# Kernel tuning notes

Hardware: AMD Instinct MI355X
Metric: run time of the kernel (lower is better)

The kernel has to match this reference:

```python
import jax, jax.numpy as jnp
import numpy as np

N, K, H, E, HEADS, MULT = 10000, 32, 128, 128, 8, 2
HD = H // HEADS


def _ln(x, g, b):
    m = jnp.mean(x, axis=-1, keepdims=True)
    v = jnp.var(x, axis=-1, keepdims=True)
    return (x - m) * jax.lax.rsqrt(v + 1e-5) * g + b


def setup_inputs() -> dict:
    key = jax.random.key(0)
    ks = jax.random.split(key, 40)
    s = 0.05
    inp = {
        "node_features": jax.random.normal(ks[0], (N, H), jnp.float32),
        "edge_features": jax.random.normal(ks[1], (N, K, H), jnp.float32),
        "edge_attr": jax.random.normal(ks[2], (N, K, E), jnp.float32),
        "neighbor_list": jax.random.randint(ks[3], (N, K), 0, N),
        "num_valid": jax.random.randint(ks[4], (N,), 1, K + 1),
        # edge_linear: E -> H (with activation)
        "W_edge": jax.random.normal(ks[5], (E, H), jnp.float32) * s,
        "b_edge": jnp.zeros((H,), jnp.float32),
        # node_linear: 2H -> H (cat of center + gathered neighbor features)
        "W_node": jax.random.normal(ks[6], (2 * H, H), jnp.float32) * s,
        "b_node": jnp.zeros((H,), jnp.float32),
        # message_linear: 2H -> H
        "W_msg": jax.random.normal(ks[7], (2 * H, H), jnp.float32) * s,
        "b_msg": jnp.zeros((H,), jnp.float32),
        # multi-head attention in/out projections
        "W_qkv": jax.random.normal(ks[8], (H, 3 * H), jnp.float32) * s,
        "b_qkv": jnp.zeros((3 * H,), jnp.float32),
        "W_out": jax.random.normal(ks[9], (H, H), jnp.float32) * s,
        "b_out": jnp.zeros((H,), jnp.float32),
        # layernorms
        "g_attn": jnp.ones((H,), jnp.float32), "be_attn": jnp.zeros((H,), jnp.float32),
        "g_fn": jnp.ones((H,), jnp.float32), "be_fn": jnp.zeros((H,), jnp.float32),
        "g_fe": jnp.ones((H,), jnp.float32), "be_fe": jnp.zeros((H,), jnp.float32),
        # FFNs (node and edge), hidden = MULT*H
        "Wn1": jax.random.normal(ks[10], (H, MULT * H), jnp.float32) * s,
        "bn1": jnp.zeros((MULT * H,), jnp.float32),
        "Wn2": jax.random.normal(ks[11], (MULT * H, H), jnp.float32) * s,
        "bn2": jnp.zeros((H,), jnp.float32),
        "We1": jax.random.normal(ks[12], (H, MULT * H), jnp.float32) * s,
        "be1": jnp.zeros((MULT * H,), jnp.float32),
        "We2": jax.random.normal(ks[13], (MULT * H, H), jnp.float32) * s,
        "be2": jnp.zeros((H,), jnp.float32),
    }
    return inp


def _block(node_features, edge_features, edge_attr, neighbor_list, mask,
           W_edge, b_edge, W_node, b_node, W_msg, b_msg,
           W_qkv, b_qkv, W_out, b_out,
           g_attn, be_attn, g_fn, be_fn, g_fe, be_fe,
           Wn1, bn1, Wn2, bn2, We1, be1, We2, be2):
    act = jax.nn.gelu
    # --- pre-attention norm on nodes ---
    node_hidden = _ln(node_features, g_attn, be_attn)                 # [N,H]
    # --- graph attention: gather -> MLPs -> local windowed attention -> scatter ---
    edge_hidden = act(jnp.einsum('nke,eh->nkh', edge_attr, W_edge) + b_edge)   # [N,K,H]
    nbr = node_hidden[neighbor_list]                                   # [N,K,H] gather
    center = jnp.broadcast_to(node_hidden[:, None, :], nbr.shape)      # [N,K,H]
    node_cat = jnp.concatenate([center, nbr], axis=-1)                 # [N,K,2H]
    node_hid = act(jnp.einsum('nkf,fh->nkh', node_cat, W_node) + b_node)
    msg = act(jnp.einsum('nkf,fh->nkh',
                         jnp.concatenate([edge_hidden, node_hid], axis=-1),
                         W_msg) + b_msg)                               # [N,K,H]
    # multi-head self-attention per node over its K neighbors, key padding mask
    qkv = jnp.einsum('nkh,hf->nkf', msg, W_qkv) + b_qkv                # [N,K,3H]
    q, k, v = jnp.split(qkv, 3, axis=-1)
    q = q.reshape(N, K, HEADS, HD)
    k = k.reshape(N, K, HEADS, HD)
    v = v.reshape(N, K, HEADS, HD)
    scores = jnp.einsum('nqhd,nkhd->nhqk', q, k) / np.sqrt(HD)         # [N,heads,K,K]
    scores = jnp.where(mask[:, None, None, :], scores, jnp.float32(-1e9))
    attn = jax.nn.softmax(scores, axis=-1)
    ctx = jnp.einsum('nhqk,nkhd->nqhd', attn, v).reshape(N, K, H)
    edge_out = jnp.einsum('nkh,hf->nkf', ctx, W_out) + b_out           # [N,K,H]
    # masked scatter-aggregate back to nodes
    node_out = jnp.sum(edge_out * mask[:, :, None], axis=1)            # [N,H]
    # residuals
    node_features = node_out + node_features
    edge_features = edge_out + edge_features
    # --- FFN block ---
    nh = _ln(node_features, g_fn, be_fn)
    eh = _ln(edge_features, g_fe, be_fe)
    nh = act(nh @ Wn1 + bn1) @ Wn2 + bn2
    eh = jnp.einsum('nkf,fh->nkh', act(jnp.einsum('nkh,hf->nkf', eh, We1) + be1), We2) + be2
    return node_features + nh, edge_features + eh


def reference(node_features, edge_features, edge_attr, neighbor_list, num_valid,
              W_edge, b_edge, W_node, b_node, W_msg, b_msg,
              W_qkv, b_qkv, W_out, b_out,
              g_attn, be_attn, g_fn, be_fn, g_fe, be_fe,
              Wn1, bn1, Wn2, bn2, We1, be1, We2, be2):
    mask = jnp.arange(K)[None, :] < num_valid[:, None]                 # [N,K] bool
    return _block(node_features, edge_features, edge_attr, neighbor_list, mask,
                  W_edge, b_edge, W_node, b_node, W_msg, b_msg,
                  W_qkv, b_qkv, W_out, b_out,
                  g_attn, be_attn, g_fn, be_fn, g_fe, be_fe,
                  Wn1, bn1, Wn2, bn2, We1, be1, We2, be2)
```

## Files before the change

### kernel.cpp

```cpp
#include <hip/hip_runtime.h>
#include <hip/hip_bf16.h>
#include <cstddef>

#define N_NODES 10000
#define KNBR 32
#define HDIM 128
#define NHEADS 8

using short8 = __attribute__((ext_vector_type(8))) short;
using short4v = __attribute__((ext_vector_type(4))) short;
using f32x4 = __attribute__((ext_vector_type(4))) float;

__device__ __forceinline__ f32x4 mfma16(short8 a, short8 b, f32x4 c) {
  return __builtin_amdgcn_mfma_f32_16x16x32_bf16(a, b, c, 0, 0, 0);
}

__device__ __forceinline__ short f2bf(float f) {
  __hip_bfloat16 h = __float2bfloat16(f);
  return __builtin_bit_cast(short, h);
}
__device__ __forceinline__ float bf2f(short s) {
  unsigned u = ((unsigned)(unsigned short)s) << 16;
  return __builtin_bit_cast(float, u);
}

__device__ __forceinline__ float gelu_f(float x) {
  float a = 0.7978845608028654f * fmaf(0.044715f * x, x * x, x);
  float e = __expf(2.0f * a);
  return 0.5f * x * (2.0f - 2.0f / (e + 1.0f));
}

__device__ __forceinline__ short4v pack4f(float a, float b, float c, float d) {
  short4v v; v[0] = f2bf(a); v[1] = f2bf(b); v[2] = f2bf(c); v[3] = f2bf(d);
  return v;
}
__device__ __forceinline__ short4v pack_gelu4(f32x4 acc, float4 bb) {
  return pack4f(gelu_f(acc[0] + bb.x), gelu_f(acc[1] + bb.y),
                gelu_f(acc[2] + bb.z), gelu_f(acc[3] + bb.w));
}

__device__ __forceinline__ short8 ld_sw128(const short* b, int r, int ch) {
  return *(const short8*)(b + r * 128 + (((ch ^ (r & 7))) << 3));
}
__device__ __forceinline__ short8 ld_sw256(const short* b, int r, int ch) {
  return *(const short8*)(b + r * 256 + (((ch ^ (r & 7))) << 3));
}
__device__ __forceinline__ void st_sw128(short* b, int r, int col, short v) {
  b[r * 128 + ((((col >> 3) ^ (r & 7))) << 3) + (col & 7)] = v;
}
__device__ __forceinline__ void st_sw128_v4(short* b, int r, int colb, short4v v) {
  *(short4v*)(b + r * 128 + ((((colb >> 3) ^ (r & 7))) << 3) + (colb & 7)) = v;
}
__device__ __forceinline__ void st_sw256_v4(short* b, int r, int colb, short4v v) {
  *(short4v*)(b + r * 256 + ((((colb >> 3) ^ (r & 7))) << 3) + (colb & 7)) = v;
}

template <int MT, int NT, int KS, typename ALoad, typename Epi>
__device__ __forceinline__ void wgemm(ALoad aload, const short* __restrict__ Bt,
                                      Epi epi) {
  const int lane = threadIdx.x & 63;
  const int lm = lane & 15, lq = lane >> 4;
  f32x4 acc[MT][NT];
#pragma unroll
  for (int mt = 0; mt < MT; ++mt)
#pragma unroll
    for (int nt = 0; nt < NT; ++nt) acc[mt][nt] = {0.f, 0.f, 0.f, 0.f};
#pragma unroll
  for (int k = 0; k < KS; ++k) {
    short8 a[MT];
#pragma unroll
    for (int mt = 0; mt < MT; ++mt) a[mt] = aload(mt * 16 + lm, k, lq);
#pragma unroll
    for (int nt = 0; nt < NT; ++nt) {
      short8 b = *(const short8*)(Bt + (nt * 16 + lm) * (KS * 32) + k * 32 + lq * 8);
#pragma unroll
      for (int mt = 0; mt < MT; ++mt) acc[mt][nt] = mfma16(a[mt], b, acc[mt][nt]);
    }
  }
#pragma unroll
  for (int mt = 0; mt < MT; ++mt)
#pragma unroll
    for (int nt = 0; nt < NT; ++nt) epi(mt, nt, acc[mt][nt]);
}

template <int MT, int NT, int KS, typename ALoad, typename Epi>
__device__ __forceinline__ void wgemm_t(ALoad aload, const short* __restrict__ Bt,
                                        Epi epi) {
  const int lane = threadIdx.x & 63;
  const int lm = lane & 15, lq = lane >> 4;
  f32x4 acc[MT][NT];
#pragma unroll
  for (int mt = 0; mt < MT; ++mt)
#pragma unroll
    for (int nt = 0; nt < NT; ++nt) acc[mt][nt] = {0.f, 0.f, 0.f, 0.f};
#pragma unroll
  for (int k = 0; k < KS; ++k) {
    short8 a[MT];
#pragma unroll
    for (int mt = 0; mt < MT; ++mt) a[mt] = aload(mt * 16 + lm, k, lq);
#pragma unroll
    for (int nt = 0; nt < NT; ++nt) {
      short8 b = *(const short8*)(Bt + (nt * 16 + lm) * (KS * 32) + k * 32 + lq * 8);
#pragma unroll
      for (int mt = 0; mt < MT; ++mt) acc[mt][nt] = mfma16(b, a[mt], acc[mt][nt]);
    }
  }
#pragma unroll
  for (int mt = 0; mt < MT; ++mt)
#pragma unroll
    for (int nt = 0; nt < NT; ++nt) epi(mt, nt, acc[mt][nt]);
}

struct WSrc { const float* p[9]; };

__global__ void wprep_kernel(WSrc ws, short* __restrict__ dst) {
  const int cum[10] = {0, 16384, 49152, 81920, 131072, 147456, 180224, 212992, 245760, 278528};
  const int Ks[9] = {128, 256, 256, 128, 128, 128, 256, 128, 256};
  const int Ns[9] = {128, 128, 128, 384, 128, 256, 128, 256, 128};
  int eg = blockIdx.x * 256 + threadIdx.x;
  int id = 0;
#pragma unroll
  for (int i = 0; i < 8; ++i) id += (eg >= cum[i + 1]) ? 1 : 0;
  int e = eg - cum[id];
  int K = Ks[id];
  int n = (K == 128) ? (e >> 7) : (e >> 8);
  int k = e - n * K;
  dst[eg] = f2bf(ws.p[id][k * Ns[id] + n]);
}

__global__ __launch_bounds__(256) void ln_in_kernel(
    const float* __restrict__ in, const float* __restrict__ g,
    const float* __restrict__ be, short* __restrict__ out) {
  __shared__ float scr[32 * 8 * 2 + 64];
  const int tid = threadIdx.x;
  const int r = tid >> 3, j = tid & 7;
  const int base = blockIdx.x * 32;
  const int rg = base + r;
  const bool valid = rg < N_NODES;
  float4 v[4];
#pragma unroll
  for (int i = 0; i < 4; ++i)
    v[i] = valid ? ((const float4*)(in + (size_t)rg * 128 + j * 16))[i]
                 : make_float4(0.f, 0.f, 0.f, 0.f);
  float s = 0.f, s2 = 0.f;
#pragma unroll
  for (int i = 0; i < 4; ++i) {
    s += v[i].x + v[i].y + v[i].z + v[i].w;
    s2 = fmaf(v[i].x, v[i].x, s2); s2 = fmaf(v[i].y, v[i].y, s2);
    s2 = fmaf(v[i].z, v[i].z, s2); s2 = fmaf(v[i].w, v[i].w, s2);
  }
  scr[r * 8 + j] = s;
  scr[256 + r * 8 + j] = s2;
  __syncthreads();
  if (tid < 32) {
    float ss = 0.f, q2 = 0.f;
#pragma unroll
    for (int i = 0; i < 8; ++i) { ss += scr[tid * 8 + i]; q2 += scr[256 + tid * 8 + i]; }
    float mn = ss * (1.f / 128.f);
    float vr = fmaf(-mn, mn, q2 * (1.f / 128.f));
    scr[512 + tid] = mn;
    scr[544 + tid] = rsqrtf(vr + 1e-5f);
  }
  __syncthreads();
  if (!valid) return;
  float mn = scr[512 + r], rs = scr[544 + r];
  short8 o[2];
#pragma unroll
  for (int i = 0; i < 4; ++i) {
    int c0 = j * 16 + i * 4;
    float4 gg = *(const float4*)(g + c0);
    float4 bb = *(const float4*)(be + c0);
    float* vf = (float*)&v[i];
    float* gf = (float*)&gg;
    float* bf = (float*)&bb;
#pragma unroll
    for (int e = 0; e < 4; ++e)
      o[i >> 1][(i & 1) * 4 + e] = f2bf(fmaf((vf[e] - mn) * rs, gf[e], bf[e]));
  }
  *(short8*)(out + (size_t)rg * 128 + j * 16) = o[0];
  *(short8*)(out + (size_t)rg * 128 + j * 16 + 8) = o[1];
}

__global__ __launch_bounds__(256, 3) void egab_main(
    const float* __restrict__ nf, const float* __restrict__ ef,
    const float* __restrict__ ea, const int* __restrict__ nlist,
    const int* __restrict__ nvalid,
    const float* __restrict__ b_edge, const float* __restrict__ b_node,
    const float* __restrict__ b_msg, const float* __restrict__ b_qkv,
    const float* __restrict__ b_out, const float* __restrict__ g_fe,
    const float* __restrict__ be_fe, const float* __restrict__ be1,
    const float* __restrict__ be2,
    const short* __restrict__ WtE, const short* __restrict__ WtN,
    const short* __restrict__ WtM, const short* __restrict__ WtQ,
    const short* __restrict__ WtO, const short* __restrict__ WtE1,
    const short* __restrict__ WtE2, const short* __restrict__ nh_bf,
    float* __restrict__ out_node, float* __restrict__ out_edge) {
  __shared__ short lds[16384];
  short* R0 = lds;
  short* R1 = lds + 4096;
  short* R2 = lds + 8192;
  short* R3 = lds + 12288;

  const int tid = threadIdx.x;
  const int w = tid >> 6;
  const int lane = tid & 63;
  const int lm = lane & 15, lq = lane >> 4;
  const int base = blockIdx.x;
  const int n0 = w * 32;

  {
    const float* eap = ea + (size_t)base * 4096;
    int r = tid >> 3;
    int sg = tid & 7;
#pragma unroll
    for (int j = 0; j < 2; ++j) {
      int ch = sg * 2 + j;
      float4 fa = ((const float4*)eap)[r * 32 + ch * 2];
      float4 fb = ((const float4*)eap)[r * 32 + ch * 2 + 1];
      short8 v = {f2bf(fa.x), f2bf(fa.y), f2bf(fa.z), f2bf(fa.w),
                  f2bf(fb.x), f2bf(fb.y), f2bf(fb.z), f2bf(fb.w)};
      *(short8*)(R0 + r * 128 + ((ch ^ (r & 7)) << 3)) = v;
    }
    int idx = nlist[base * KNBR + r];
    const short* srow = nh_bf + (size_t)idx * 128;
#pragma unroll
    for (int j = 0; j < 2; ++j) {
      int ch = sg * 2 + j;
      short8 v = *(const short8*)(srow + ch * 8);
      *(short8*)(R1 + r * 128 + ((ch ^ (r & 7)) << 3)) = v;
    }
  }
  __syncthreads();

  wgemm_t<2, 2, 4>(
      [&](int r, int k, int q) { return ld_sw128(R0, r, k * 4 + q); },
      WtE + (size_t)n0 * 128,
      [&](int mt, int nt, f32x4 acc) {
        int colb = n0 + nt * 16 + lq * 4;
        float4 bb = *(const float4*)(b_edge + colb);
        st_sw128_v4(R2, mt * 16 + lm, colb, pack_gelu4(acc, bb));
      });
  wgemm_t<2, 2, 8>(
      [&](int r, int k, int q) {
        if (k < 4)
          return *(const short8*)(nh_bf + (size_t)base * 128 + k * 32 + q * 8);
        return ld_sw128(R1, r, (k - 4) * 4 + q);
      },
      WtN + (size_t)n0 * 256,
      [&](int mt, int nt, f32x4 acc) {
        int colb = n0 + nt * 16 + lq * 4;
        float4 bb = *(const float4*)(b_node + colb);
        st_sw128_v4(R3, mt * 16 + lm, colb, pack_gelu4(acc, bb));
      });
  __syncthreads();

  wgemm_t<2, 2, 8>(
      [&](int r, int k, int q) {
        if (k < 4) return ld_sw128(R2, r, k * 4 + q);
        return ld_sw128(R3, r, (k - 4) * 4 + q);
      },
      WtM + (size_t)n0 * 256,
      [&](int mt, int nt, f32x4 acc) {
        int colb = n0 + nt * 16 + lq * 4;
        float4 bb = *(const float4*)(b_msg + colb);
        st_sw128_v4(R0, mt * 16 + lm, colb, pack_gelu4(acc, bb));
      });
  __syncthreads();

  {
    auto ald = [&](int r, int k, int q) { return ld_sw128(R0, r, k * 4 + q); };
    wgemm_t<2, 2, 4>(
        ald, WtQ + (size_t)(w * 32) * 128,
        [&](int mt, int nt, f32x4 acc) {
          int colb = w * 32 + nt * 16 + lq * 4;
          float4 bb = *(const float4*)(b_qkv + colb);
          int h = colb >> 4;
          *(short4v*)(R1 + h * 512 + (mt * 16 + lm) * 16 + (colb & 15)) =
              pack4f(acc[0] + bb.x, acc[1] + bb.y, acc[2] + bb.z, acc[3] + bb.w);
        });
    wgemm_t<2, 2, 4>(
        ald, WtQ + (size_t)(128 + w * 32) * 128,
        [&](int mt, int nt, f32x4 acc) {
          int colb = 128 + w * 32 + nt * 16 + lq * 4;
          float4 bb = *(const float4*)(b_qkv + colb);
          int h = (colb - 128) >> 4;
          *(short4v*)(R2 + h * 512 + (mt * 16 + lm) * 16 + (colb & 15)) =
              pack4f(acc[0] + bb.x, acc[1] + bb.y, acc[2] + bb.z, acc[3] + bb.w);
        });
    wgemm<2, 2, 4>(
        ald, WtQ + (size_t)(256 + w * 32) * 128,
        [&](int mt, int nt, f32x4 acc) {
          int c = 256 + w * 32 + nt * 16;
          float bb = b_qkv[c + lm];
          int rv = (c - 256) + lm;
          short4v pv;
#pragma unroll
          for (int rr = 0; rr < 4; ++rr) pv[rr] = f2bf(acc[rr] + bb);
          int m = mt * 16 + lq * 4;
          int chv = m >> 3;
          *(short4v*)(R3 + rv * 32 + ((chv ^ (rv & 3)) << 3) + (m & 7)) = pv;
        });
  }
  __syncthreads();

  {
    const short8 zz = {0, 0, 0, 0, 0, 0, 0, 0};
    const f32x4 z4 = {0.f, 0.f, 0.f, 0.f};
    const int nvv = nvalid[base];
#pragma unroll
    for (int it = 0; it < 2; ++it) {
      int h = (it << 2) | w;
      short* qh = R1 + h * 512;
      short* kh = R2 + h * 512;
      short8 bk[2];
#pragma unroll
      for (int nt = 0; nt < 2; ++nt)
        bk[nt] = (lq < 2) ? *(const short8*)(kh + (nt * 16 + lm) * 16 + lq * 8) : zz;
      float sc[2][2][4];
#pragma unroll
      for (int mt = 0; mt < 2; ++mt) {
        short8 aq = (lq < 2) ? *(const short8*)(qh + (mt * 16 + lm) * 16 + lq * 8) : zz;
#pragma unroll
        for (int nt = 0; nt < 2; ++nt) {
          f32x4 s = mfma16(aq, bk[nt], z4);
#pragma unroll
          for (int rr = 0; rr < 4; ++rr) {
            float x = s[rr] * 0.25f;
            if (nt * 16 + lm >= nvv) x = -1e9f;
            sc[mt][nt][rr] = x;
          }
        }
      }
#pragma unroll
      for (int mt = 0; mt < 2; ++mt)
#pragma unroll
        for (int rr = 0; rr < 4; ++rr) {
          float x0 = sc[mt][0][rr], x1 = sc[mt][1][rr];
          float mx = fmaxf(x0, x1);
          mx = fmaxf(mx, __shfl_xor(mx, 1, 16));
          mx = fmaxf(mx, __shfl_xor(mx, 2, 16));
          mx = fmaxf(mx, __shfl_xor(mx, 4, 16));
          mx = fmaxf(mx, __shfl_xor(mx, 8, 16));
          float e0 = __expf(x0 - mx), e1 = __expf(x1 - mx);
          float sm = e0 + e1;
          sm += __shfl_xor(sm, 1, 16);
          sm += __shfl_xor(sm, 2, 16);
          sm += __shfl_xor(sm, 4, 16);
          sm += __shfl_xor(sm, 8, 16);
          float ri = 1.f / sm;
          int row = mt * 16 + lq * 4 + rr;
          qh[row * 16 + lm] = f2bf(e0 * ri);
          kh[row * 16 + lm] = f2bf(e1 * ri);
        }
#pragma unroll
      for (int mt = 0; mt < 2; ++mt) {
        const short* psrc = (lq < 2) ? qh : kh;
        short8 pa = *(const short8*)(psrc + (mt * 16 + lm) * 16 + (lq & 1) * 8);
        int rv = h * 16 + lm;
        short8 vb = *(const short8*)(R3 + rv * 32 + ((lq ^ (rv & 3)) << 3));
        f32x4 c = mfma16(pa, vb, z4);
#pragma unroll
        for (int rr = 0; rr < 4; ++rr)
          st_sw128(R0, mt * 16 + lq * 4 + rr, h * 16 + lm, f2bf(c[rr]));
      }
    }
  }
  __syncthreads();

  {
    int nv = nvalid[base];
    float nsum[2] = {0.f, 0.f};
    wgemm<2, 2, 4>(
        [&](int r, int k, int q) { return ld_sw128(R0, r, k * 4 + q); },
        WtO + (size_t)n0 * 128,
        [&](int mt, int nt, f32x4 acc) {
          int col = n0 + nt * 16 + lm;
          float bb = b_out[col];
#pragma unroll
          for (int rr = 0; rr < 4; ++rr) {
            int kk = mt * 16 + lq * 4 + rr;
            float eo = acc[rr] + bb;
            if (kk < nv) nsum[nt] += eo;
            float efv = ef[((size_t)base * KNBR + kk) * 128 + col];
            st_sw128(R1, kk, col, f2bf(eo + efv));
          }
        });
#pragma unroll
    for (int nt = 0; nt < 2; ++nt) {
      float v = nsum[nt];
      v += __shfl_xor(v, 16, 64);
      v += __shfl_xor(v, 32, 64);
      if (lq == 0) {
        int col = n0 + nt * 16 + lm;
        out_node[(size_t)base * 128 + col] =
            v + nf[(size_t)base * 128 + col];
      }
    }
  }
  __syncthreads();

  {
    float* scr = (float*)R2;
    int r = tid >> 3, sg = tid & 7;
    short8 xv[2];
    float s = 0.f, s2 = 0.f;
#pragma unroll
    for (int j = 0; j < 2; ++j) {
      int ch = sg * 2 + j;
      xv[j] = *(const short8*)(R1 + r * 128 + ((ch ^ (r & 7)) << 3));
#pragma unroll
      for (int e = 0; e < 8; ++e) {
        float x = bf2f(xv[j][e]);
        s += x;
        s2 = fmaf(x, x, s2);
      }
    }
    scr[r * 8 + sg] = s;
    scr[256 + r * 8 + sg] = s2;
    __syncthreads();
    if (tid < 32) {
      float ss = 0.f, q2 = 0.f;
#pragma unroll
      for (int i = 0; i < 8; ++i) { ss += scr[tid * 8 + i]; q2 += scr[256 + tid * 8 + i]; }
      float mn = ss * (1.f / 128.f);
      float vr = fmaf(-mn, mn, q2 * (1.f / 128.f));
      scr[512 + tid * 2] = mn;
      scr[512 + tid * 2 + 1] = rsqrtf(vr + 1e-5f);
    }
    __syncthreads();
    float mn = scr[512 + r * 2], rs = scr[512 + r * 2 + 1];
#pragma unroll
    for (int j = 0; j < 2; ++j) {
      int ch = sg * 2 + j;
      int c0 = ch * 8;
      float4 g0 = *(const float4*)(g_fe + c0);
      float4 g1 = *(const float4*)(g_fe + c0 + 4);
      float4 b0 = *(const float4*)(be_fe + c0);
      float4 b1 = *(const float4*)(be_fe + c0 + 4);
      const float* gp0 = (const float*)&g0;
      const float* gp1 = (const float*)&g1;
      const float* bp0 = (const float*)&b0;
      const float* bp1 = (const float*)&b1;
      short8 ov;
#pragma unroll
      for (int e = 0; e < 4; ++e) {
        ov[e] = f2bf(fmaf((bf2f(xv[j][e]) - mn) * rs, gp0[e], bp0[e]));
        ov[4 + e] = f2bf(fmaf((bf2f(xv[j][4 + e]) - mn) * rs, gp1[e], bp1[e]));
      }
      *(short8*)(R0 + r * 128 + ((ch ^ (r & 7)) << 3)) = ov;
    }
  }
  __syncthreads();

  {
    const int f0 = w * 64;
    wgemm_t<2, 4, 4>(
        [&](int r, int k, int q) { return ld_sw128(R0, r, k * 4 + q); },
        WtE1 + (size_t)f0 * 128,
        [&](int mt, int nt, f32x4 acc) {
          int colb = f0 + nt * 16 + lq * 4;
          float4 bb = *(const float4*)(be1 + colb);
          st_sw256_v4(R2, mt * 16 + lm, colb, pack_gelu4(acc, bb));
        });
  }
  __syncthreads();

  wgemm<2, 2, 8>(
      [&](int r, int k, int q) { return ld_sw256(R2, r, k * 4 + q); },
      WtE2 + (size_t)n0 * 256,
      [&](int mt, int nt, f32x4 acc) {
        int col = n0 + nt * 16 + lm;
        float bb = be2[col];
#pragma unroll
        for (int rr = 0; rr < 4; ++rr) {
          int m = mt * 16 + lq * 4 + rr;
          float rv = bf2f(R1[m * 128 + ((((col >> 3) ^ (m & 7))) << 3) + (col & 7)]);
          out_edge[((size_t)base * KNBR + m) * 128 + col] = rv + acc[rr] + bb;
        }
      });
}

__global__ __launch_bounds__(256, 4) void node_ffn_kernel(
    const float* __restrict__ nres, const float* __restrict__ g,
    const float* __restrict__ be, const short* __restrict__ WtN1,
    const float* __restrict__ bn1, const short* __restrict__ WtN2,
    const float* __restrict__ bn2, float* __restrict__ out) {
  __shared__ short lds[8192];
  short* EHN = lds;
  float* scr = (float*)(lds + 2048);
  short* HID = lds + 4096;

  const int tid = threadIdx.x;
  const int w = tid >> 6;
  const int lane = tid & 63;
  const int lm = lane & 15, lq = lane >> 4;
  const int base = blockIdx.x * 16;
  const int n0 = w * 32;

  {
    int r = tid >> 4, sg = tid & 15;
    bool valid = (base + r) < N_NODES;
    float xf[8];
#pragma unroll
    for (int i = 0; i < 2; ++i) {
      float4 v = valid ? ((const float4*)(nres + (size_t)(base + r) * 128 + sg * 8))[i]
                       : make_float4(0.f, 0.f, 0.f, 0.f);
      xf[i * 4] = v.x; xf[i * 4 + 1] = v.y; xf[i * 4 + 2] = v.z; xf[i * 4 + 3] = v.w;
    }
    float s = 0.f, s2 = 0.f;
#pragma unroll
    for (int i = 0; i < 8; ++i) { s += xf[i]; s2 = fmaf(xf[i], xf[i], s2); }
    scr[r * 16 + sg] = s;
    scr[256 + r * 16 + sg] = s2;
    __syncthreads();
    if (tid < 16) {
      float ss = 0.f, q2 = 0.f;
#pragma unroll
      for (int i = 0; i < 16; ++i) { ss += scr[tid * 16 + i]; q2 += scr[256 + tid * 16 + i]; }
      float mn = ss * (1.f / 128.f);
      float vr = fmaf(-mn, mn, q2 * (1.f / 128.f));
      scr[512 + tid * 2] = mn;
      scr[512 + tid * 2 + 1] = rsqrtf(vr + 1e-5f);
    }
    __syncthreads();
    float mn = scr[512 + r * 2], rs = scr[512 + r * 2 + 1];
    int c0 = sg * 8;
    short8 ov;
#pragma unroll
    for (int e = 0; e < 8; ++e)
      ov[e] = f2bf(fmaf((xf[e] - mn) * rs, g[c0 + e], be[c0 + e]));
    *(short8*)(EHN + r * 128 + ((sg ^ (r & 7)) << 3)) = ov;
  }
  __syncthreads();

  {
    const int f0 = w * 64;
    wgemm_t<1, 4, 4>(
        [&](int r, int k, int q) { return ld_sw128(EHN, r, k * 4 + q); },
        WtN1 + (size_t)f0 * 128,
        [&](int mt, int nt, f32x4 acc) {
          int colb = f0 + nt * 16 + lq * 4;
          float4 bb = *(const float4*)(bn1 + colb);
          st_sw256_v4(HID, mt * 16 + lm, colb, pack_gelu4(acc, bb));
        });
  }
  __syncthreads();

  wgemm<1, 2, 8>(
      [&](int r, int k, int q) { return ld_sw256(HID, r, k * 4 + q); },
      WtN2 + (size_t)n0 * 256,
      [&](int mt, int nt, f32x4 acc) {
        int col = n0 + nt * 16 + lm;
        float bb = bn2[col];
#pragma unroll
        for (int rr = 0; rr < 4; ++rr) {
          int m = mt * 16 + lq * 4 + rr;
          if (base + m < N_NODES) {
            float rv = nres[(size_t)(base + m) * 128 + col];
            out[(size_t)(base + m) * 128 + col] = rv + acc[rr] + bb;
          }
        }
      });
}

extern "C" void kernel_launch(void* const* d_in, const int* in_sizes, int n_in,
                              void* d_out, int out_size, void* d_ws,
                              size_t ws_size, hipStream_t stream) {
  (void)in_sizes; (void)n_in; (void)out_size; (void)ws_size;
  const float* nf = (const float*)d_in[0];
  const float* ef = (const float*)d_in[1];
  const float* ea = (const float*)d_in[2];
  const int* nlist = (const int*)d_in[3];
  const int* nvalid = (const int*)d_in[4];
  const float* W_edge = (const float*)d_in[5];
  const float* b_edge = (const float*)d_in[6];
  const float* W_node = (const float*)d_in[7];
  const float* b_node = (const float*)d_in[8];
  const float* W_msg = (const float*)d_in[9];
  const float* b_msg = (const float*)d_in[10];
  const float* W_qkv = (const float*)d_in[11];
  const float* b_qkv = (const float*)d_in[12];
  const float* W_out = (const float*)d_in[13];
  const float* b_out = (const float*)d_in[14];
  const float* g_attn = (const float*)d_in[15];
  const float* be_attn = (const float*)d_in[16];
  const float* g_fn = (const float*)d_in[17];
  const float* be_fn = (const float*)d_in[18];
  const float* g_fe = (const float*)d_in[19];
  const float* be_fe = (const float*)d_in[20];
  const float* Wn1 = (const float*)d_in[21];
  const float* bn1 = (const float*)d_in[22];
  const float* Wn2 = (const float*)d_in[23];
  const float* bn2 = (const float*)d_in[24];
  const float* We1 = (const float*)d_in[25];
  const float* be1 = (const float*)d_in[26];
  const float* We2 = (const float*)d_in[27];
  const float* be2 = (const float*)d_in[28];

  short* ws0 = (short*)d_ws;
  short* wsW = ws0 + 1280000;
  short* WtE = wsW;
  short* WtN = wsW + 16384;
  short* WtM = wsW + 49152;
  short* WtQ = wsW + 81920;
  short* WtO = wsW + 131072;
  short* WtE1 = wsW + 147456;
  short* WtE2 = wsW + 180224;
  short* WtN1 = wsW + 212992;
  short* WtN2 = wsW + 245760;

  float* out_node = (float*)d_out;
  float* out_edge = out_node + (size_t)N_NODES * 128;

  WSrc wsrc;
  wsrc.p[0] = W_edge; wsrc.p[1] = W_node; wsrc.p[2] = W_msg;
  wsrc.p[3] = W_qkv;  wsrc.p[4] = W_out;  wsrc.p[5] = We1;
  wsrc.p[6] = We2;    wsrc.p[7] = Wn1;    wsrc.p[8] = Wn2;

  wprep_kernel<<<1088, 256, 0, stream>>>(wsrc, wsW);
  ln_in_kernel<<<(N_NODES + 31) / 32, 256, 0, stream>>>(nf, g_attn, be_attn, ws0);
  egab_main<<<N_NODES, 256, 0, stream>>>(
      nf, ef, ea, nlist, nvalid, b_edge, b_node, b_msg, b_qkv, b_out, g_fe,
      be_fe, be1, be2, WtE, WtN, WtM, WtQ, WtO, WtE1, WtE2, ws0, out_node,
      out_edge);
  node_ffn_kernel<<<(N_NODES + 15) / 16, 256, 0, stream>>>(
      out_node, g_fn, be_fn, WtN1, bn1, WtN2, bn2, out_node);
}
```

Baseline: 949.7 us.

## Restructure wave GEMMs to preload A/B fragments, merge QKV projections, prefetch residuals

The wave-level GEMM helpers now load all A fragments up front and, for each output column tile, load every B fragment before running the k-chain of MFMAs into a single accumulator. This trades fewer live accumulators for more live operand registers and longer dependent MFMA chains. The three QKV projections are merged into one 2x6 GEMM per wave over a contiguous 96-column slice, with the epilogue deciding per tile whether to write Q, K or V layout, which changes how Q/K are stored (scalar strided stores). Residual edge and node features are loaded from global memory at kernel start so their latency overlaps earlier compute, at the cost of extra registers held across the whole kernel.

New measurement: 911.8 us. -4.0%, faster.

```diff
diff --git a/kernel.cpp b/kernel.cpp
--- a/kernel.cpp
+++ b/kernel.cpp
@@ -60,27 +60,25 @@
                                       Epi epi) {
   const int lane = threadIdx.x & 63;
   const int lm = lane & 15, lq = lane >> 4;
-  f32x4 acc[MT][NT];
+  short8 a[MT][KS];
 #pragma unroll
   for (int mt = 0; mt < MT; ++mt)
 #pragma unroll
-    for (int nt = 0; nt < NT; ++nt) acc[mt][nt] = {0.f, 0.f, 0.f, 0.f};
-#pragma unroll
-  for (int k = 0; k < KS; ++k) {
-    short8 a[MT];
-#pragma unroll
-    for (int mt = 0; mt < MT; ++mt) a[mt] = aload(mt * 16 + lm, k, lq);
-#pragma unroll
-    for (int nt = 0; nt < NT; ++nt) {
-      short8 b = *(const short8*)(Bt + (nt * 16 + lm) * (KS * 32) + k * 32 + lq * 8);
-#pragma unroll
-      for (int mt = 0; mt < MT; ++mt) acc[mt][nt] = mfma16(a[mt], b, acc[mt][nt]);
-    }
-  }
-#pragma unroll
-  for (int mt = 0; mt < MT; ++mt)
-#pragma unroll
-    for (int nt = 0; nt < NT; ++nt) epi(mt, nt, acc[mt][nt]);
+    for (int k = 0; k < KS; ++k) a[mt][k] = aload(mt * 16 + lm, k, lq);
+#pragma unroll
+  for (int nt = 0; nt < NT; ++nt) {
+    short8 b[KS];
+#pragma unroll
+    for (int k = 0; k < KS; ++k)
+      b[k] = *(const short8*)(Bt + (nt * 16 + lm) * (KS * 32) + k * 32 + lq * 8);
+#pragma unroll
+    for (int mt = 0; mt < MT; ++mt) {
+      f32x4 acc = {0.f, 0.f, 0.f, 0.f};
+#pragma unroll
+      for (int k = 0; k < KS; ++k) acc = mfma16(a[mt][k], b[k], acc);
+      epi(mt, nt, acc);
+    }
+  }
 }
 
 template <int MT, int NT, int KS, typename ALoad, typename Epi>
@@ -88,27 +86,25 @@
                                         Epi epi) {
   const int lane = threadIdx.x & 63;
   const int lm = lane & 15, lq = lane >> 4;
-  f32x4 acc[MT][NT];
+  short8 a[MT][KS];
 #pragma unroll
   for (int mt = 0; mt < MT; ++mt)
 #pragma unroll
-    for (int nt = 0; nt < NT; ++nt) acc[mt][nt] = {0.f, 0.f, 0.f, 0.f};
-#pragma unroll
-  for (int k = 0; k < KS; ++k) {
-    short8 a[MT];
-#pragma unroll
-    for (int mt = 0; mt < MT; ++mt) a[mt] = aload(mt * 16 + lm, k, lq);
-#pragma unroll
-    for (int nt = 0; nt < NT; ++nt) {
-      short8 b = *(const short8*)(Bt + (nt * 16 + lm) * (KS * 32) + k * 32 + lq * 8);
-#pragma unroll
-      for (int mt = 0; mt < MT; ++mt) acc[mt][nt] = mfma16(b, a[mt], acc[mt][nt]);
-    }
-  }
-#pragma unroll
-  for (int mt = 0; mt < MT; ++mt)
-#pragma unroll
-    for (int nt = 0; nt < NT; ++nt) epi(mt, nt, acc[mt][nt]);
+    for (int k = 0; k < KS; ++k) a[mt][k] = aload(mt * 16 + lm, k, lq);
+#pragma unroll
+  for (int nt = 0; nt < NT; ++nt) {
+    short8 b[KS];
+#pragma unroll
+    for (int k = 0; k < KS; ++k)
+      b[k] = *(const short8*)(Bt + (nt * 16 + lm) * (KS * 32) + k * 32 + lq * 8);
+#pragma unroll
+    for (int mt = 0; mt < MT; ++mt) {
+      f32x4 acc = {0.f, 0.f, 0.f, 0.f};
+#pragma unroll
+      for (int k = 0; k < KS; ++k) acc = mfma16(b[k], a[mt][k], acc);
+      epi(mt, nt, acc);
+    }
+  }
 }
 
 struct WSrc { const float* p[9]; };
@@ -207,6 +203,21 @@
   const int lm = lane & 15, lq = lane >> 4;
   const int base = blockIdx.x;
   const int n0 = w * 32;
+
+  float efr[2][2][4];
+  float nfr[2];
+#pragma unroll
+  for (int mt = 0; mt < 2; ++mt)
+#pragma unroll
+    for (int nt = 0; nt < 2; ++nt)
+#pragma unroll
+      for (int rr = 0; rr < 4; ++rr)
+        efr[mt][nt][rr] =
+            ef[((size_t)base * KNBR + mt * 16 + lq * 4 + rr) * 128 + n0 +
+               nt * 16 + lm];
+#pragma unroll
+  for (int nt = 0; nt < 2; ++nt)
+    nfr[nt] = nf[(size_t)base * 128 + n0 + nt * 16 + lm];
 
   {
     const float* eap = ea + (size_t)base * 4096;
@@ -268,37 +279,28 @@
   __syncthreads();
 
   {
-    auto ald = [&](int r, int k, int q) { return ld_sw128(R0, r, k * 4 + q); };
-    wgemm_t<2, 2, 4>(
-        ald, WtQ + (size_t)(w * 32) * 128,
+    const int q0 = w * 96;
+    wgemm<2, 6, 4>(
+        [&](int r, int k, int q) { return ld_sw128(R0, r, k * 4 + q); },
+        WtQ + (size_t)q0 * 128,
         [&](int mt, int nt, f32x4 acc) {
-          int colb = w * 32 + nt * 16 + lq * 4;
-          float4 bb = *(const float4*)(b_qkv + colb);
-          int h = colb >> 4;
-          *(short4v*)(R1 + h * 512 + (mt * 16 + lm) * 16 + (colb & 15)) =
-              pack4f(acc[0] + bb.x, acc[1] + bb.y, acc[2] + bb.z, acc[3] + bb.w);
-        });
-    wgemm_t<2, 2, 4>(
-        ald, WtQ + (size_t)(128 + w * 32) * 128,
-        [&](int mt, int nt, f32x4 acc) {
-          int colb = 128 + w * 32 + nt * 16 + lq * 4;
-          float4 bb = *(const float4*)(b_qkv + colb);
-          int h = (colb - 128) >> 4;
-          *(short4v*)(R2 + h * 512 + (mt * 16 + lm) * 16 + (colb & 15)) =
-              pack4f(acc[0] + bb.x, acc[1] + bb.y, acc[2] + bb.z, acc[3] + bb.w);
-        });
-    wgemm<2, 2, 4>(
-        ald, WtQ + (size_t)(256 + w * 32) * 128,
-        [&](int mt, int nt, f32x4 acc) {
-          int c = 256 + w * 32 + nt * 16;
+          int c = q0 + nt * 16;
           float bb = b_qkv[c + lm];
-          int rv = (c - 256) + lm;
-          short4v pv;
-#pragma unroll
-          for (int rr = 0; rr < 4; ++rr) pv[rr] = f2bf(acc[rr] + bb);
           int m = mt * 16 + lq * 4;
-          int chv = m >> 3;
-          *(short4v*)(R3 + rv * 32 + ((chv ^ (rv & 3)) << 3) + (m & 7)) = pv;
+          if (c < 256) {
+            short* dst = (c < 128 ? R1 + ((c >> 4) * 32) * 16
+                                  : R2 + (((c - 128) >> 4) * 32) * 16);
+#pragma unroll
+            for (int rr = 0; rr < 4; ++rr)
+              dst[(m + rr) * 16 + lm] = f2bf(acc[rr] + bb);
+          } else {
+            int rv = (c - 256) + lm;
+            short4v pv;
+#pragma unroll
+            for (int rr = 0; rr < 4; ++rr) pv[rr] = f2bf(acc[rr] + bb);
+            int chv = m >> 3;
+            *(short4v*)(R3 + rv * 32 + ((chv ^ (rv & 3)) << 3) + (m & 7)) = pv;
+          }
         });
   }
   __syncthreads();
@@ -381,8 +383,7 @@
             int kk = mt * 16 + lq * 4 + rr;
             float eo = acc[rr] + bb;
             if (kk < nv) nsum[nt] += eo;
-            float efv = ef[((size_t)base * KNBR + kk) * 128 + col];
-            st_sw128(R1, kk, col, f2bf(eo + efv));
+            st_sw128(R1, kk, col, f2bf(eo + efr[mt][nt][rr]));
           }
         });
 #pragma unroll
@@ -392,8 +393,7 @@
       v += __shfl_xor(v, 32, 64);
       if (lq == 0) {
         int col = n0 + nt * 16 + lm;
-        out_node[(size_t)base * 128 + col] =
-            v + nf[(size_t)base * 128 + col];
+        out_node[(size_t)base * 128 + col] = v + nfr[nt];
       }
     }
   }
```
